# Performance work log

Hardware: AMD Instinct MI355X
Metric: run time of the kernel (lower is better)

The kernel has to match this reference:

```python
import jax, jax.numpy as jnp
import numpy as np

N = 2048       # x_dim (input features)
M = 2048       # y_dim (output features)
R0 = 1024      # components in table 0 (knn table)
D_K = 1024     # key encoder embed dim
D_V = 1024     # val encoder embed dim
BATCH = 512
ISTA_ALPHA = 1.0
ISTA_MAXITER = 5


def _ortho_encoder(key, n, d):
    # get_embedding_matrix with ortho=True: QR of (s,s) gaussian, take [:n,:d]
    s = max(n, d)
    q = jnp.linalg.qr(jax.random.normal(key, (s, s), dtype=jnp.float32))[0]
    return q[:n, :d]


def setup_inputs() -> dict:
    key = jax.random.key(0)
    kw, kk, kv, kx = jax.random.split(key, 4)
    W = jax.random.normal(kw, (N, M), dtype=jnp.float32) / np.float32(np.sqrt(N))
    # torch: V, S, U = svd(W); U = U.T  -> V = left vecs (n,k), U = right vecs (m,k)
    Usvd, S, Vh = jnp.linalg.svd(W, full_matrices=False)
    V = Usvd          # (n, k)
    Ur = Vh.T         # (m, k)
    key_enc = _ortho_encoder(kk, N, D_K)   # (n, d_k)
    val_enc = _ortho_encoder(kv, M, D_V)   # (m, d_v)
    # table 0: knn table over components [0:R0]
    keys_t0 = V[:, :R0].T @ key_enc        # (R0, d_k)
    vals_t0 = Ur[:, :R0].T @ val_enc       # (R0, d_v)
    scales_t0 = S[:R0][:, None]            # (R0, 1)
    # table 1: plain low-rank table over components [R0:]
    keys_t1 = V[:, R0:]                    # (n, R1)
    vals_t1 = Ur[:, R0:]                   # (m, R1)
    scales_t1 = S[R0:][:, None]            # (R1, 1)
    x = jax.random.normal(kx, (BATCH, N), dtype=jnp.float32)
    return {"x": x, "key_enc": key_enc, "val_enc": val_enc,
            "keys_t0": keys_t0, "vals_t0": vals_t0, "scales_t0": scales_t0,
            "keys_t1": keys_t1, "vals_t1": vals_t1, "scales_t1": scales_t1}


def _soft(x, t):
    return jnp.sign(x) * jnp.maximum(jnp.abs(x) - t, 0.0)


def reference(x, key_enc, val_enc, keys_t0, vals_t0, scales_t0,
              keys_t1, vals_t1, scales_t1):
    # --- table 0: knn path (batched; original looped over batch samples) ---
    q = x @ key_enc                        # (B, d_k)
    alphas = q @ keys_t0.T                 # (B, R0)
    betas = alphas * scales_t0.T           # (B, R0)
    yb = betas @ vals_t0                   # (B, d_v)
    # ISTA: min ||yb - z @ val_enc||^2 + alpha*||z||_1, step=1 (val_enc has
    # orthonormal columns so Lipschitz const of grad is 1)
    z = yb @ val_enc.T                     # z0, (B, m)
    for _ in range(ISTA_MAXITER):
        z = _soft(z + (yb - z @ val_enc) @ val_enc.T, ISTA_ALPHA)
    y = z                                  # knn path assigns y[b,:] = yh
    # --- table 1: low-rank path (accumulates) ---
    alphas2 = x @ keys_t1                  # (B, R1)
    betas2 = alphas2 * scales_t1.T         # (B, R1)
    y = y + betas2 @ vals_t1.T             # (B, m)
    return y
```

## Files before the change

kernel.cpp:

```cpp
#include <hip/hip_runtime.h>


typedef _Float16 f16x8 __attribute__((ext_vector_type(8)));
typedef _Float16 f16x4 __attribute__((ext_vector_type(4)));
typedef float f32x4 __attribute__((ext_vector_type(4)));

enum { EPI_H, EPI_QW, EPI_SPLIT, EPI_SOFT, EPI_ZQ, EPI_FINAL };

typedef const __attribute__((address_space(1))) void* gas_ptr;
typedef __attribute__((address_space(3))) void* las_ptr;

__device__ __forceinline__ void gload16(const void* g, void* l) {
  __builtin_amdgcn_global_load_lds((gas_ptr)g, (las_ptr)l, 16, 0, 0);
}

__device__ __forceinline__ float softt(float t) {
  float s = fabsf(t) - 1.0f;
  s = s > 0.0f ? s : 0.0f;
  return copysignf(s, t);
}

__global__ __launch_bounds__(256) void convAll(
    const float* __restrict__ e0, const float* __restrict__ e1,
    const float* __restrict__ e2, const float* __restrict__ e3,
    _Float16* __restrict__ o0, _Float16* __restrict__ o1,
    _Float16* __restrict__ o2, _Float16* __restrict__ o3,
    const float* __restrict__ s1, const float* __restrict__ s2,
    const float4* __restrict__ pa, f16x4* __restrict__ qa, int na,
    const float4* __restrict__ pb, f16x4* __restrict__ qb, int nb,
    const float4* __restrict__ pc, f16x4* __restrict__ qc, int nc) {
  const int z = blockIdx.z;
  if (z == 4) {
    const int total = na + nb + nc;
    const int bid = blockIdx.y * 32 + blockIdx.x;
    const int nthr = 2048 * 256;
    for (int i = bid * 256 + threadIdx.y * 32 + threadIdx.x; i < total;
         i += nthr) {
      const float4* s;
      f16x4* d;
      int j = i;
      if (j < na) {
        s = pa; d = qa;
      } else if ((j -= na) < nb) {
        s = pb; d = qb;
      } else {
        j -= nb; s = pc; d = qc;
      }
      float4 v = s[j];
      f16x4 h = {(_Float16)v.x, (_Float16)v.y, (_Float16)v.z, (_Float16)v.w};
      d[j] = h;
    }
    return;
  }
  const float* in = z == 0 ? e0 : z == 1 ? e1 : z == 2 ? e2 : e3;
  _Float16* out = z == 0 ? o0 : z == 1 ? o1 : z == 2 ? o2 : o3;
  const int R = (z < 2) ? 2048 : 1024;
  const int C = 1024;
  const int mode = z == 1 ? 1 : z == 2 ? 2 : 0;
  const float* sv = z == 1 ? s1 : s2;
  __shared__ float t[32][33];
  const int tx = threadIdx.x, ty = threadIdx.y;
  const int c0 = blockIdx.x * 32, r0 = blockIdx.y * 32;
  if (r0 >= R) return;
#pragma unroll
  for (int i = 0; i < 32; i += 8)
    t[ty + i][tx] = in[(size_t)(r0 + ty + i) * C + c0 + tx];
  __syncthreads();
#pragma unroll
  for (int i = 0; i < 32; i += 8) {
    float v = t[tx][ty + i];
    if (mode == 1) v *= sv[c0 + ty + i];
    if (mode == 2) v *= sv[r0 + tx];
    out[(size_t)(c0 + ty + i) * R + r0 + tx] = (_Float16)v;
  }
}

template <int EPI>
__global__ __launch_bounds__(512) void gemmk(
    const _Float16* __restrict__ A, const _Float16* __restrict__ B,
    const int N, const int K, const float* caux, const float* caux2,
    const float* dgv, float* dgout, float* outf,
    _Float16* __restrict__ outh, _Float16* __restrict__ outh2) {
  __shared__ __align__(16) _Float16 sm[40960];
  const int tid = threadIdx.x;
  const int lane = tid & 63;
  const int w = tid >> 6;
  const int wr = (w >> 1) & 1;
  const int wc = w & 1;
  const int wk = w >> 2;
  const int brow = blockIdx.y << 6;
  const int bcol = blockIdx.x << 6;

  const int srow = lane >> 3;
  const int scol = ((lane & 7) ^ srow) << 3;
  const int a15 = lane & 15;
  const int hi = lane >> 4;
  const int l7 = lane & 7;

  const _Float16* apg = A + (size_t)(brow + (w << 3) + srow) * K + scol;
  const _Float16* bpg = B + (size_t)(bcol + (w << 3) + srow) * K + scol;
  const int ldst = w << 9;

  int raddr[2], baddr[2];
#pragma unroll
  for (int mi = 0; mi < 2; ++mi) {
    int ra = (wr << 5) + (mi << 4) + a15;
    int ca = ((wk << 2) + hi) ^ l7;
    raddr[mi] = ra * 64 + (ca << 3);
  }
#pragma unroll
  for (int ni = 0; ni < 2; ++ni) {
    int rb = (wc << 5) + (ni << 4) + a15;
    int cb = ((wk << 2) + hi) ^ l7;
    baddr[ni] = rb * 64 + (cb << 3);
  }

  f32x4 acc[2][2] = {};
  const int nK = K >> 6;

#pragma unroll
  for (int p = 0; p < 3; ++p) {
    gload16(apg + (p << 6), sm + p * 4096 + ldst);
    gload16(bpg + (p << 6), sm + 20480 + p * 4096 + ldst);
  }

  int bi = 0, bs = 3;
  for (int kt = 0; kt < nK; ++kt) {
    if (kt + 3 < nK) {
      gload16(apg + ((size_t)(kt + 3) << 6), sm + bs * 4096 + ldst);
      gload16(bpg + ((size_t)(kt + 3) << 6), sm + 20480 + bs * 4096 + ldst);
    }
    const int rem = nK - 1 - kt;
    if (rem >= 3)
      asm volatile("s_waitcnt vmcnt(6)" ::: "memory");
    else if (rem == 2)
      asm volatile("s_waitcnt vmcnt(4)" ::: "memory");
    else if (rem == 1)
      asm volatile("s_waitcnt vmcnt(2)" ::: "memory");
    else
      asm volatile("s_waitcnt vmcnt(0)" ::: "memory");
    __builtin_amdgcn_s_barrier();
    __builtin_amdgcn_sched_barrier(0);
    const _Float16* Ab = sm + bi * 4096;
    const _Float16* Bb = sm + 20480 + bi * 4096;
    f16x8 av[2], bv[2];
    av[0] = *(const f16x8*)(Ab + raddr[0]);
    av[1] = *(const f16x8*)(Ab + raddr[1]);
    bv[0] = *(const f16x8*)(Bb + baddr[0]);
    bv[1] = *(const f16x8*)(Bb + baddr[1]);
#pragma unroll
    for (int mi = 0; mi < 2; ++mi)
#pragma unroll
      for (int ni = 0; ni < 2; ++ni)
        acc[mi][ni] = __builtin_amdgcn_mfma_f32_16x16x32_f16(
            av[mi], bv[ni], acc[mi][ni], 0, 0, 0);
    bi = bi == 4 ? 0 : bi + 1;
    bs = bs == 4 ? 0 : bs + 1;
  }
  __syncthreads();

  float* scr = (float*)sm;
  const int rbase = ((w & 3) * 64 + lane) * 16;
  if (wk == 1) {
#pragma unroll
    for (int mi = 0; mi < 2; ++mi)
#pragma unroll
      for (int ni = 0; ni < 2; ++ni)
        *(f32x4*)(scr + rbase + ((mi * 2 + ni) << 2)) = acc[mi][ni];
  }
  __syncthreads();
  if (wk == 1) return;
#pragma unroll
  for (int mi = 0; mi < 2; ++mi)
#pragma unroll
    for (int ni = 0; ni < 2; ++ni)
      acc[mi][ni] += *(const f32x4*)(scr + rbase + ((mi * 2 + ni) << 2));

#pragma unroll
  for (int mi = 0; mi < 2; ++mi) {
#pragma unroll
    for (int ni = 0; ni < 2; ++ni) {
#pragma unroll
      for (int r = 0; r < 4; ++r) {
        const int row = brow + (wr << 5) + (mi << 4) + (hi << 2) + r;
        const int col = bcol + (wc << 5) + (ni << 4) + a15;
        const float v = acc[mi][ni][r];
        const size_t idx = (size_t)row * N + col;
        if constexpr (EPI == EPI_H) {
          outh[idx] = (_Float16)v;
        } else if constexpr (EPI == EPI_QW) {
          if (col < 2048) {
            if (row == col) {
              dgout[row] = 1.0f - v;
              outh[(size_t)row * 2048 + col] = (_Float16)0.0f;
            } else {
              outh[(size_t)row * 2048 + col] = (_Float16)(-v);
            }
          } else {
            outh2[(size_t)row * 1024 + (col - 2048)] = (_Float16)v;
          }
        } else if constexpr (EPI == EPI_SPLIT) {
          if (col < 1024)
            outh[(size_t)row * 1024 + col] = (_Float16)v;
          else
            outh2[(size_t)row * 1024 + (col - 1024)] = (_Float16)v;
        } else if constexpr (EPI == EPI_SOFT) {
          outf[idx] = v;
          float s = softt(v);
          caux[0]; (void)0;
          ((float*)caux2)[idx] = s;
          outh[idx] = (_Float16)s;
        } else if constexpr (EPI == EPI_ZQ) {
          float t = caux[idx] + dgv[col] * caux2[idx] + v;
          float s = softt(t);
          outf[idx] = s;
          outh[idx] = (_Float16)s;
        } else {
          outf[idx] = caux[idx] + v;
        }
      }
    }
  }
}

extern "C" void kernel_launch(void* const* d_in, const int* in_sizes, int n_in,
                              void* d_out, int out_size, void* d_ws,
                              size_t ws_size, hipStream_t stream) {
  const float* x = (const float*)d_in[0];
  const float* key_enc = (const float*)d_in[1];
  const float* val_enc = (const float*)d_in[2];
  const float* keys_t0 = (const float*)d_in[3];
  const float* vals_t0 = (const float*)d_in[4];
  const float* scales_t0 = (const float*)d_in[5];
  const float* keys_t1 = (const float*)d_in[6];
  const float* vals_t1 = (const float*)d_in[7];
  const float* scales_t1 = (const float*)d_in[8];

  _Float16* wsh = (_Float16*)d_ws;
  _Float16* ve_h = wsh;
  _Float16* w0_h = wsh + 2097152;
  _Float16* vt1_h = wsh + 3145728;
  _Float16* w0pT = wsh + 5242880;
  _Float16* Bcat = wsh + 7340032;
  _Float16* qoff = Bcat;
  _Float16* x_h = wsh + 11534336;
  float* dg = (float*)x_h;
  _Float16* kt0s = wsh + 12582912;
  _Float16* zh_A = kt0s;
  _Float16* vt0T = wsh + 13631488;
  _Float16* zh_B = vt0T;
  _Float16* q_h = wsh + 14680064;
  _Float16* be2_h = wsh + 15204352;
  float* z0_f = (float*)(wsh + 15728640);
  float* z_f = z0_f + 1048576;

  convAll<<<dim3(32, 64, 5), dim3(32, 8), 0, stream>>>(
      key_enc, keys_t1, keys_t0, vals_t0, Bcat, Bcat + 2097152, kt0s, vt0T,
      scales_t1, scales_t0, (const float4*)x, (f16x4*)x_h, 262144,
      (const float4*)val_enc, (f16x4*)ve_h, 524288, (const float4*)vals_t1,
      (f16x4*)vt1_h, 524288);

  gemmk<EPI_SPLIT><<<dim3(32, 8), 512, 0, stream>>>(
      x_h, Bcat, 2048, 2048, nullptr, nullptr, nullptr, nullptr, nullptr, q_h,
      be2_h);
  gemmk<EPI_H><<<dim3(16, 16), 512, 0, stream>>>(
      kt0s, vt0T, 1024, 1024, nullptr, nullptr, nullptr, nullptr, nullptr,
      w0_h, nullptr);
  gemmk<EPI_QW><<<dim3(48, 32), 512, 0, stream>>>(
      ve_h, ve_h, 3072, 1024, nullptr, nullptr, nullptr, dg, nullptr, qoff,
      w0pT);
  gemmk<EPI_SOFT><<<dim3(32, 8), 512, 0, stream>>>(
      q_h, w0pT, 2048, 1024, nullptr, (const float*)z_f, nullptr, nullptr,
      z0_f, zh_A, nullptr);
  gemmk<EPI_ZQ><<<dim3(32, 8), 512, 0, stream>>>(
      zh_A, qoff, 2048, 2048, z0_f, z_f, dg, nullptr, z_f, zh_B, nullptr);
  gemmk<EPI_ZQ><<<dim3(32, 8), 512, 0, stream>>>(
      zh_B, qoff, 2048, 2048, z0_f, z_f, dg, nullptr, z_f, zh_A, nullptr);
  gemmk<EPI_ZQ><<<dim3(32, 8), 512, 0, stream>>>(
      zh_A, qoff, 2048, 2048, z0_f, z_f, dg, nullptr, z_f, zh_B, nullptr);
  gemmk<EPI_ZQ><<<dim3(32, 8), 512, 0, stream>>>(
      zh_B, qoff, 2048, 2048, z0_f, z_f, dg, nullptr, z_f, zh_A, nullptr);
  gemmk<EPI_FINAL><<<dim3(32, 8), 512, 0, stream>>>(
      be2_h, vt1_h, 2048, 1024, z_f, nullptr, nullptr, nullptr, (float*)d_out,
      nullptr, nullptr);
}
```

Measured before the change: 128.0 us.

## Merge independent GEMMs into one launch, reassociate W0 product, fuse final ISTA step

Replaces the per-GEMM launches with a shared 64x64 tile device routine using 256 threads (4 waves, 2-way K split, 4-stage/2-ahead pipeline) and groups the three independent setup GEMMs (QOFF, SPLIT, W0) into one grid. The val_enc product is reassociated: instead of computing ve*ve^T over 3072 columns, w0pT is formed by a separate ve x W0 GEMM. The last ISTA iteration and the low-rank output GEMM are fused in one kernel. The aim is fewer launches and less per-launch tail idle time, at the cost of an extra dependent launch (kW0p) and changed tiling.

```diff
diff --git a/kernel.cpp b/kernel.cpp
--- a/kernel.cpp
+++ b/kernel.cpp
@@ -5,7 +5,7 @@
 typedef _Float16 f16x4 __attribute__((ext_vector_type(4)));
 typedef float f32x4 __attribute__((ext_vector_type(4)));
 
-enum { EPI_H, EPI_QW, EPI_SPLIT, EPI_SOFT, EPI_ZQ, EPI_FINAL };
+enum { EPI_H, EPI_QOFF, EPI_SPLIT, EPI_SOFT, EPI_ZQ, EPI_ZQF, EPI_FINAL };
 
 typedef const __attribute__((address_space(1))) void* gas_ptr;
 typedef __attribute__((address_space(3))) void* las_ptr;
@@ -76,151 +76,208 @@
 }
 
 template <int EPI>
-__global__ __launch_bounds__(512) void gemmk(
-    const _Float16* __restrict__ A, const _Float16* __restrict__ B,
-    const int N, const int K, const float* caux, const float* caux2,
-    const float* dgv, float* dgout, float* outf,
-    _Float16* __restrict__ outh, _Float16* __restrict__ outh2) {
-  __shared__ __align__(16) _Float16 sm[40960];
-  const int tid = threadIdx.x;
+__device__ __forceinline__ void gtile(
+    const _Float16* __restrict__ A, int lda, const _Float16* __restrict__ B,
+    int ldb, int nK, int N, int brow, int bcol, const float* __restrict__ dgv,
+    float* __restrict__ dgout, float* __restrict__ fA, float* __restrict__ fB,
+    _Float16* __restrict__ oh, _Float16* __restrict__ oh2,
+    float* __restrict__ ofin, _Float16* sm, int tid) {
   const int lane = tid & 63;
   const int w = tid >> 6;
-  const int wr = (w >> 1) & 1;
-  const int wc = w & 1;
-  const int wk = w >> 2;
-  const int brow = blockIdx.y << 6;
-  const int bcol = blockIdx.x << 6;
-
+  const int wr = w & 1;
+  const int wk = w >> 1;
   const int srow = lane >> 3;
   const int scol = ((lane & 7) ^ srow) << 3;
   const int a15 = lane & 15;
   const int hi = lane >> 4;
   const int l7 = lane & 7;
 
-  const _Float16* apg = A + (size_t)(brow + (w << 3) + srow) * K + scol;
-  const _Float16* bpg = B + (size_t)(bcol + (w << 3) + srow) * K + scol;
-  const int ldst = w << 9;
-
-  int raddr[2], baddr[2];
-#pragma unroll
-  for (int mi = 0; mi < 2; ++mi) {
-    int ra = (wr << 5) + (mi << 4) + a15;
-    int ca = ((wk << 2) + hi) ^ l7;
-    raddr[mi] = ra * 64 + (ca << 3);
-  }
-#pragma unroll
-  for (int ni = 0; ni < 2; ++ni) {
-    int rb = (wc << 5) + (ni << 4) + a15;
-    int cb = ((wk << 2) + hi) ^ l7;
-    baddr[ni] = rb * 64 + (cb << 3);
-  }
-
-  f32x4 acc[2][2] = {};
-  const int nK = K >> 6;
-
-#pragma unroll
-  for (int p = 0; p < 3; ++p) {
-    gload16(apg + (p << 6), sm + p * 4096 + ldst);
-    gload16(bpg + (p << 6), sm + 20480 + p * 4096 + ldst);
-  }
-
-  int bi = 0, bs = 3;
+  const _Float16* apg = A + (size_t)(brow + (w << 4) + srow) * lda + scol;
+  const _Float16* bpg = B + (size_t)(bcol + (w << 4) + srow) * ldb + scol;
+  _Float16* AB = sm;
+  _Float16* BB = sm + 16384;
+  const int ldstA = w << 10;
+
+  const int ca = ((wk << 2) + hi) ^ l7;
+  int raddr[2], baddr[4];
+#pragma unroll
+  for (int mi = 0; mi < 2; ++mi)
+    raddr[mi] = ((wr << 5) + (mi << 4) + a15) * 64 + (ca << 3);
+#pragma unroll
+  for (int ni = 0; ni < 4; ++ni)
+    baddr[ni] = ((ni << 4) + a15) * 64 + (ca << 3);
+
+  f32x4 acc[2][4] = {};
+
+  __syncthreads();
+
+#pragma unroll
+  for (int p = 0; p < 2; ++p) {
+    gload16(apg + p * 64, AB + p * 4096 + ldstA);
+    gload16(apg + p * 64 + (size_t)8 * lda, AB + p * 4096 + ldstA + 512);
+    gload16(bpg + p * 64, BB + p * 4096 + ldstA);
+    gload16(bpg + p * 64 + (size_t)8 * ldb, BB + p * 4096 + ldstA + 512);
+  }
+
   for (int kt = 0; kt < nK; ++kt) {
-    if (kt + 3 < nK) {
-      gload16(apg + ((size_t)(kt + 3) << 6), sm + bs * 4096 + ldst);
-      gload16(bpg + ((size_t)(kt + 3) << 6), sm + 20480 + bs * 4096 + ldst);
+    if (kt + 2 < nK) {
+      const int bf = (kt + 2) & 3;
+      const int co = (kt + 2) << 6;
+      gload16(apg + co, AB + bf * 4096 + ldstA);
+      gload16(apg + co + (size_t)8 * lda, AB + bf * 4096 + ldstA + 512);
+      gload16(bpg + co, BB + bf * 4096 + ldstA);
+      gload16(bpg + co + (size_t)8 * ldb, BB + bf * 4096 + ldstA + 512);
     }
     const int rem = nK - 1 - kt;
-    if (rem >= 3)
-      asm volatile("s_waitcnt vmcnt(6)" ::: "memory");
-    else if (rem == 2)
+    if (rem >= 2)
+      asm volatile("s_waitcnt vmcnt(8)" ::: "memory");
+    else if (rem == 1)
       asm volatile("s_waitcnt vmcnt(4)" ::: "memory");
-    else if (rem == 1)
-      asm volatile("s_waitcnt vmcnt(2)" ::: "memory");
     else
       asm volatile("s_waitcnt vmcnt(0)" ::: "memory");
     __builtin_amdgcn_s_barrier();
     __builtin_amdgcn_sched_barrier(0);
-    const _Float16* Ab = sm + bi * 4096;
-    const _Float16* Bb = sm + 20480 + bi * 4096;
-    f16x8 av[2], bv[2];
+    const _Float16* Ab = AB + (kt & 3) * 4096;
+    const _Float16* Bb = BB + (kt & 3) * 4096;
+    f16x8 av[2], bv[4];
     av[0] = *(const f16x8*)(Ab + raddr[0]);
     av[1] = *(const f16x8*)(Ab + raddr[1]);
     bv[0] = *(const f16x8*)(Bb + baddr[0]);
     bv[1] = *(const f16x8*)(Bb + baddr[1]);
+    bv[2] = *(const f16x8*)(Bb + baddr[2]);
+    bv[3] = *(const f16x8*)(Bb + baddr[3]);
 #pragma unroll
     for (int mi = 0; mi < 2; ++mi)
 #pragma unroll
-      for (int ni = 0; ni < 2; ++ni)
+      for (int ni = 0; ni < 4; ++ni)
         acc[mi][ni] = __builtin_amdgcn_mfma_f32_16x16x32_f16(
             av[mi], bv[ni], acc[mi][ni], 0, 0, 0);
-    bi = bi == 4 ? 0 : bi + 1;
-    bs = bs == 4 ? 0 : bs + 1;
-  }
+  }
+
   __syncthreads();
-
   float* scr = (float*)sm;
-  const int rbase = ((w & 3) * 64 + lane) * 16;
+  const int sl = (wr << 6) + lane;
   if (wk == 1) {
 #pragma unroll
     for (int mi = 0; mi < 2; ++mi)
 #pragma unroll
-      for (int ni = 0; ni < 2; ++ni)
-        *(f32x4*)(scr + rbase + ((mi * 2 + ni) << 2)) = acc[mi][ni];
+      for (int ni = 0; ni < 4; ++ni)
+#pragma unroll
+        for (int r = 0; r < 4; ++r)
+          scr[(((mi << 2) + ni) * 4 + r) * 128 + sl] = acc[mi][ni][r];
   }
   __syncthreads();
-  if (wk == 1) return;
-#pragma unroll
-  for (int mi = 0; mi < 2; ++mi)
-#pragma unroll
-    for (int ni = 0; ni < 2; ++ni)
-      acc[mi][ni] += *(const f32x4*)(scr + rbase + ((mi * 2 + ni) << 2));
-
-#pragma unroll
-  for (int mi = 0; mi < 2; ++mi) {
-#pragma unroll
-    for (int ni = 0; ni < 2; ++ni) {
-#pragma unroll
-      for (int r = 0; r < 4; ++r) {
-        const int row = brow + (wr << 5) + (mi << 4) + (hi << 2) + r;
-        const int col = bcol + (wc << 5) + (ni << 4) + a15;
-        const float v = acc[mi][ni][r];
-        const size_t idx = (size_t)row * N + col;
-        if constexpr (EPI == EPI_H) {
-          outh[idx] = (_Float16)v;
-        } else if constexpr (EPI == EPI_QW) {
-          if (col < 2048) {
+  if (wk == 0) {
+#pragma unroll
+    for (int mi = 0; mi < 2; ++mi) {
+#pragma unroll
+      for (int ni = 0; ni < 4; ++ni) {
+#pragma unroll
+        for (int r = 0; r < 4; ++r) {
+          const float v =
+              acc[mi][ni][r] + scr[(((mi << 2) + ni) * 4 + r) * 128 + sl];
+          const int row = brow + (wr << 5) + (mi << 4) + (hi << 2) + r;
+          const int col = bcol + (ni << 4) + a15;
+          const size_t idx = (size_t)row * N + col;
+          if constexpr (EPI == EPI_H) {
+            oh[idx] = (_Float16)v;
+          } else if constexpr (EPI == EPI_QOFF) {
             if (row == col) {
               dgout[row] = 1.0f - v;
-              outh[(size_t)row * 2048 + col] = (_Float16)0.0f;
+              oh[idx] = (_Float16)0.0f;
             } else {
-              outh[(size_t)row * 2048 + col] = (_Float16)(-v);
+              oh[idx] = (_Float16)(-v);
             }
+          } else if constexpr (EPI == EPI_SPLIT) {
+            if (col < 1024)
+              oh[(size_t)row * 1024 + col] = (_Float16)v;
+            else
+              oh2[(size_t)row * 1024 + (col - 1024)] = (_Float16)v;
+          } else if constexpr (EPI == EPI_SOFT) {
+            fA[idx] = v;
+            float s = softt(v);
+            fB[idx] = s;
+            oh[idx] = (_Float16)s;
+          } else if constexpr (EPI == EPI_ZQ) {
+            float t = fA[idx] + dgv[col] * fB[idx] + v;
+            float s = softt(t);
+            fB[idx] = s;
+            oh[idx] = (_Float16)s;
+          } else if constexpr (EPI == EPI_ZQF) {
+            float t = fA[idx] + dgv[col] * fB[idx] + v;
+            fB[idx] = softt(t);
           } else {
-            outh2[(size_t)row * 1024 + (col - 2048)] = (_Float16)v;
+            ofin[idx] = fB[idx] + v;
           }
-        } else if constexpr (EPI == EPI_SPLIT) {
-          if (col < 1024)
-            outh[(size_t)row * 1024 + col] = (_Float16)v;
-          else
-            outh2[(size_t)row * 1024 + (col - 1024)] = (_Float16)v;
-        } else if constexpr (EPI == EPI_SOFT) {
-          outf[idx] = v;
-          float s = softt(v);
-          caux[0]; (void)0;
-          ((float*)caux2)[idx] = s;
-          outh[idx] = (_Float16)s;
-        } else if constexpr (EPI == EPI_ZQ) {
-          float t = caux[idx] + dgv[col] * caux2[idx] + v;
-          float s = softt(t);
-          outf[idx] = s;
-          outh[idx] = (_Float16)s;
-        } else {
-          outf[idx] = caux[idx] + v;
         }
       }
     }
   }
+}
+
+struct WS {
+  const _Float16 *ve, *vt1, *w0pT_r, *Bcat, *qoff_r, *x, *kt0s, *vt0T, *w0_r,
+      *q_r, *be2;
+  _Float16 *w0pT_w, *qoff_w, *w0_w, *q_w, *be2_w, *zhA, *zhB;
+  float *z0, *zf, *dg;
+};
+
+__global__ __launch_bounds__(256, 2) void kD2(WS p) {
+  __shared__ __align__(16) _Float16 sm[32768];
+  const int tid = threadIdx.x;
+  const int bid = blockIdx.x;
+  if (bid < 1024) {
+    gtile<EPI_QOFF>(p.ve, 1024, p.ve, 1024, 16, 2048, (bid >> 5) << 6,
+                    (bid & 31) << 6, nullptr, p.dg, nullptr, nullptr, p.qoff_w,
+                    nullptr, nullptr, sm, tid);
+  } else if (bid < 1280) {
+    const int i = bid - 1024;
+    gtile<EPI_SPLIT>(p.x, 2048, p.Bcat, 2048, 32, 2048, (i >> 5) << 6,
+                     (i & 31) << 6, nullptr, nullptr, nullptr, nullptr, p.q_w,
+                     p.be2_w, nullptr, sm, tid);
+  } else {
+    const int i = bid - 1280;
+    gtile<EPI_H>(p.kt0s, 1024, p.vt0T, 1024, 16, 1024, (i >> 4) << 6,
+                 (i & 15) << 6, nullptr, nullptr, nullptr, nullptr, p.w0_w,
+                 nullptr, nullptr, sm, tid);
+  }
+}
+
+__global__ __launch_bounds__(256, 2) void kW0p(WS p) {
+  __shared__ __align__(16) _Float16 sm[32768];
+  const int bid = blockIdx.x;
+  gtile<EPI_H>(p.ve, 1024, p.w0_r, 1024, 16, 1024, (bid >> 4) << 6,
+               (bid & 15) << 6, nullptr, nullptr, nullptr, nullptr, p.w0pT_w,
+               nullptr, nullptr, sm, threadIdx.x);
+}
+
+__global__ __launch_bounds__(256, 2) void kC2(WS p) {
+  __shared__ __align__(16) _Float16 sm[32768];
+  const int bid = blockIdx.x;
+  gtile<EPI_SOFT>(p.q_r, 1024, p.w0pT_r, 1024, 16, 2048, (bid >> 5) << 6,
+                  (bid & 31) << 6, nullptr, nullptr, p.z0, p.zf, p.zhA,
+                  nullptr, nullptr, sm, threadIdx.x);
+}
+
+template <bool AB>
+__global__ __launch_bounds__(256, 2) void kZQ(WS p) {
+  __shared__ __align__(16) _Float16 sm[32768];
+  const int bid = blockIdx.x;
+  gtile<EPI_ZQ>(AB ? p.zhA : p.zhB, 2048, p.qoff_r, 2048, 32, 2048,
+                (bid >> 5) << 6, (bid & 31) << 6, p.dg, nullptr, p.z0, p.zf,
+                AB ? p.zhB : p.zhA, nullptr, nullptr, sm, threadIdx.x);
+}
+
+__global__ __launch_bounds__(256, 2) void kZQF(WS p, float* out) {
+  __shared__ __align__(16) _Float16 sm[32768];
+  const int bid = blockIdx.x;
+  const int brow = (bid >> 5) << 6, bcol = (bid & 31) << 6;
+  gtile<EPI_ZQF>(p.zhB, 2048, p.qoff_r, 2048, 32, 2048, brow, bcol, p.dg,
+                 nullptr, p.z0, p.zf, nullptr, nullptr, nullptr, sm,
+                 threadIdx.x);
+  gtile<EPI_FINAL>(p.be2, 1024, p.vt1, 1024, 16, 2048, brow, bcol, nullptr,
+                   nullptr, nullptr, p.zf, nullptr, nullptr, out, sm,
+                   threadIdx.x);
 }
 
 extern "C" void kernel_launch(void* const* d_in, const int* in_sizes, int n_in,
@@ -236,51 +293,42 @@
   const float* vals_t1 = (const float*)d_in[7];
   const float* scales_t1 = (const float*)d_in[8];
 
-  _Float16* wsh = (_Float16*)d_ws;
-  _Float16* ve_h = wsh;
-  _Float16* w0_h = wsh + 2097152;
-  _Float16* vt1_h = wsh + 3145728;
-  _Float16* w0pT = wsh + 5242880;
-  _Float16* Bcat = wsh + 7340032;
-  _Float16* qoff = Bcat;
-  _Float16* x_h = wsh + 11534336;
-  float* dg = (float*)x_h;
-  _Float16* kt0s = wsh + 12582912;
-  _Float16* zh_A = kt0s;
-  _Float16* vt0T = wsh + 13631488;
-  _Float16* zh_B = vt0T;
-  _Float16* q_h = wsh + 14680064;
-  _Float16* be2_h = wsh + 15204352;
-  float* z0_f = (float*)(wsh + 15728640);
-  float* z_f = z0_f + 1048576;
+  constexpr size_t M1 = 1048576;
+  _Float16* ws = (_Float16*)d_ws;
+  _Float16* ve_h = ws;
+  _Float16* vt1_h = ws + 2 * M1;
+  _Float16* w0pT = ws + 4 * M1;
+  _Float16* Bcat = ws + 6 * M1;
+  _Float16* zhA = ws + 6 * M1;
+  float* z0_f = (float*)(ws + 7 * M1);
+  _Float16* zhB = ws + 9 * M1;
+  _Float16* qoff = ws + 10 * M1;
+  _Float16* x_h = ws + 14 * M1;
+  _Float16* kt0s = ws + 15 * M1;
+  float* z_f = (float*)(ws + 15 * M1);
+  _Float16* vt0T = ws + 16 * M1;
+  _Float16* w0 = ws + 17 * M1;
+  _Float16* q_h = ws + 18 * M1;
+  _Float16* be2 = ws + 18 * M1 + 524288;
+  float* dg = (float*)(ws + 19 * M1);
+
+  WS p;
+  p.ve = ve_h; p.vt1 = vt1_h; p.w0pT_r = w0pT; p.w0pT_w = w0pT;
+  p.Bcat = Bcat; p.qoff_r = qoff; p.qoff_w = qoff; p.x = x_h;
+  p.kt0s = kt0s; p.vt0T = vt0T; p.w0_r = w0; p.w0_w = w0;
+  p.q_r = q_h; p.q_w = q_h; p.be2 = be2; p.be2_w = be2;
+  p.zhA = zhA; p.zhB = zhB; p.z0 = z0_f; p.zf = z_f; p.dg = dg;
 
   convAll<<<dim3(32, 64, 5), dim3(32, 8), 0, stream>>>(
-      key_enc, keys_t1, keys_t0, vals_t0, Bcat, Bcat + 2097152, kt0s, vt0T,
+      key_enc, keys_t1, keys_t0, vals_t0, Bcat, Bcat + 2 * M1, kt0s, vt0T,
       scales_t1, scales_t0, (const float4*)x, (f16x4*)x_h, 262144,
       (const float4*)val_enc, (f16x4*)ve_h, 524288, (const float4*)vals_t1,
       (f16x4*)vt1_h, 524288);
-
-  gemmk<EPI_SPLIT><<<dim3(32, 8), 512, 0, stream>>>(
-      x_h, Bcat, 2048, 2048, nullptr, nullptr, nullptr, nullptr, nullptr, q_h,
-      be2_h);
-  gemmk<EPI_H><<<dim3(16, 16), 512, 0, stream>>>(
-      kt0s, vt0T, 1024, 1024, nullptr, nullptr, nullptr, nullptr, nullptr,
-      w0_h, nullptr);
-  gemmk<EPI_QW><<<dim3(48, 32), 512, 0, stream>>>(
-      ve_h, ve_h, 3072, 1024, nullptr, nullptr, nullptr, dg, nullptr, qoff,
-      w0pT);
-  gemmk<EPI_SOFT><<<dim3(32, 8), 512, 0, stream>>>(
-      q_h, w0pT, 2048, 1024, nullptr, (const float*)z_f, nullptr, nullptr,
-      z0_f, zh_A, nullptr);
-  gemmk<EPI_ZQ><<<dim3(32, 8), 512, 0, stream>>>(
-      zh_A, qoff, 2048, 2048, z0_f, z_f, dg, nullptr, z_f, zh_B, nullptr);
-  gemmk<EPI_ZQ><<<dim3(32, 8), 512, 0, stream>>>(
-      zh_B, qoff, 2048, 2048, z0_f, z_f, dg, nullptr, z_f, zh_A, nullptr);
-  gemmk<EPI_ZQ><<<dim3(32, 8), 512, 0, stream>>>(
-      zh_A, qoff, 2048, 2048, z0_f, z_f, dg, nullptr, z_f, zh_B, nullptr);
-  gemmk<EPI_ZQ><<<dim3(32, 8), 512, 0, stream>>>(
-      zh_B, qoff, 2048, 2048, z0_f, z_f, dg, nullptr, z_f, zh_A, nullptr);
-  gemmk<EPI_FINAL><<<dim3(32, 8), 512, 0, stream>>>(
-      be2_h, vt1_h, 2048, 1024, z_f, nullptr, nullptr, nullptr, (float*)d_out,
-      nullptr, nullptr);
-}
+  kD2<<<1536, 256, 0, stream>>>(p);
+  kW0p<<<512, 256, 0, stream>>>(p);
+  kC2<<<256, 256, 0, stream>>>(p);
+  kZQ<true><<<256, 256, 0, stream>>>(p);
+  kZQ<false><<<256, 256, 0, stream>>>(p);
+  kZQ<true><<<256, 256, 0, stream>>>(p);
+  kZQF<<<256, 256, 0, stream>>>(p, (float*)d_out);
+}
```

Result: faster. 120.7 us (-5.7%).
